# Optimization experiments

Measured on AMD Instinct MI355X. Metric: run time of the kernel, lower is better.

## Reference

```python
import jax, jax.numpy as jnp
import numpy as np

N_COMPRESS = 2048
N_EXPAND_QK = 1024
N_EXPAND_V = 1024
TOPK_C, TOPK_QK, TOPK_V = 8, 4, 6


def _topk_sparsify(w, k):
    # top-k along last dim, scatter back, renormalize (matches torch scatter_ path)
    vals, idx = jax.lax.top_k(w, k)                      # [B,k]
    rows = jnp.arange(w.shape[0])[:, None]
    sparse = jnp.zeros_like(w).at[rows, idx].set(vals)   # [B,N]
    return sparse / (sparse.sum(axis=-1, keepdims=True) + 1e-8)


def setup_inputs() -> dict:
    key = jax.random.key(0)
    k0, k1, k2, k3 = jax.random.split(key, 4)
    B, S, D, DS = 4, 4096, 2048, 64
    total = N_COMPRESS + N_EXPAND_QK + N_EXPAND_V
    return {
        "x": jax.random.normal(k0, (B, S, D), jnp.float32),
        "importance": jax.random.uniform(k1, (B, S), jnp.float32),
        "W": jax.random.normal(k2, (D, DS), jnp.float32) * 0.02,
        "b": jnp.zeros((DS,), jnp.float32),
        "neuron_emb": jax.random.normal(k3, (total, DS), jnp.float32) * 0.02,
    }


def reference(x, importance, W, b, neuron_emb):
    # projection (dropout is identity in eval mode)
    h = x @ W + b                                             # [B,S,ds]
    # cosine logits against unit-norm neuron embeddings
    emb_n = neuron_emb / jnp.linalg.norm(neuron_emb, axis=-1, keepdims=True)
    all_logits = jnp.einsum('bsd,nd->bsn', h, emb_n)          # [B,S,total]
    lC = all_logits[..., :N_COMPRESS]
    lQK = all_logits[..., N_COMPRESS:N_COMPRESS + N_EXPAND_QK]
    lV = all_logits[..., N_COMPRESS + N_EXPAND_QK:]
    pC = jax.nn.softmax(lC, axis=-1)
    pQK = jax.nn.softmax(lQK, axis=-1)   # expand_Q and expand_K share the slice (eval: identical)
    pV = jax.nn.softmax(lV, axis=-1)
    # importance-weighted pooling to per-batch dense routing weights
    dC = jnp.einsum('bs,bsn->bn', importance, pC)
    dQK = jnp.einsum('bs,bsn->bn', importance, pQK)
    dV = jnp.einsum('bs,bsn->bn', importance, pV)
    wC = _topk_sparsify(dC, TOPK_C)
    wQ = _topk_sparsify(dQK, TOPK_QK)
    wK = _topk_sparsify(dQK, TOPK_QK)
    wV = _topk_sparsify(dV, TOPK_V)
    # concat the four routing-weight outputs: [B, 2048+1024+1024+1024]
    return jnp.concatenate([wC, wQ, wK, wV], axis=-1)
```

## Files before the change

### kernel.cpp

```cpp
#include <hip/hip_runtime.h>
#include <math.h>

#define D_IN   2048

typedef __bf16 bf16x8 __attribute__((ext_vector_type(8)));
typedef float  f32x4  __attribute__((ext_vector_type(4)));

#define mfma16 __builtin_amdgcn_mfma_f32_16x16x32_bf16

__global__ __launch_bounds__(256) void k_prep(const float* __restrict__ emb,
                                              const float* __restrict__ W,
                                              __bf16* __restrict__ e_hi,
                                              __bf16* __restrict__ e_lo,
                                              __bf16* __restrict__ wt_hi,
                                              __bf16* __restrict__ wt_lo,
                                              float* __restrict__ dacc) {
    int blk = blockIdx.x, t = threadIdx.x;
    if (blk < 1024) {
        int gid  = blk * 256 + t;
        int row  = gid >> 6;
        int lane = gid & 63;
        float v  = emb[row * 64 + lane];
        float ss = v * v;
#pragma unroll
        for (int m = 32; m >= 1; m >>= 1) ss += __shfl_xor(ss, m);
        float nv = v / sqrtf(ss);
        __bf16 hb = (__bf16)nv;
        e_hi[row * 64 + lane] = hb;
        e_lo[row * 64 + lane] = (__bf16)(nv - (float)hb);
    } else if (blk < 1536) {
        int gid = (blk - 1024) * 256 + t;
        int c   = gid >> 11;
        int k   = gid & 2047;
        float v = W[k * 64 + c];
        __bf16 hb = (__bf16)v;
        wt_hi[c * 2048 + k] = hb;
        wt_lo[c * 2048 + k] = (__bf16)(v - (float)hb);
    } else {
        dacc[(blk - 1536) * 256 + t] = 0.f;
    }
}

__global__ __launch_bounds__(512, 4) void k_fused(
        const float* __restrict__ x,
        const __bf16* __restrict__ wt_hi, const __bf16* __restrict__ wt_lo,
        const float* __restrict__ bias,
        const __bf16* __restrict__ e_hi, const __bf16* __restrict__ e_lo,
        const float* __restrict__ imp, float* __restrict__ dacc) {
    __shared__ float  h_acc[32][66];
    __shared__ __bf16 hb_hi[32][64];
    __shared__ __bf16 hb_lo[32][64];
    __shared__ float  zs[8][4][8];

    int t    = threadIdx.x;
    int wave = t >> 6;
    int lane = t & 63;
    int l15  = lane & 15;
    int kg   = lane >> 4;
    int row0 = blockIdx.x * 32;
    const f32x4 z4 = {0.f, 0.f, 0.f, 0.f};

    for (int i = t; i < 32 * 66; i += 512) ((float*)h_acc)[i] = 0.f;
    __syncthreads();

    {
        f32x4 hacc[2][4];
#pragma unroll
        for (int rt = 0; rt < 2; ++rt)
#pragma unroll
            for (int ct = 0; ct < 4; ++ct) hacc[rt][ct] = z4;
        int kb0 = wave * 256;
        const float* xr0 = x + (size_t)(row0 + l15) * D_IN + kb0 + kg * 8;
        const float* xr1 = xr0 + 16 * D_IN;
        float4 xe0, xe1, xe2, xe3, xo0, xo1, xo2, xo3;

#define LDX(B, KS) { B##0 = *(const float4*)(xr0 + (KS) * 32); \
                     B##1 = *(const float4*)(xr0 + (KS) * 32 + 4); \
                     B##2 = *(const float4*)(xr1 + (KS) * 32); \
                     B##3 = *(const float4*)(xr1 + (KS) * 32 + 4); }
#define CVT8(DH, DL, V0, V1) { \
    float av[8] = {V0.x, V0.y, V0.z, V0.w, V1.x, V1.y, V1.z, V1.w}; \
    _Pragma("unroll") for (int j = 0; j < 8; ++j) { \
        __bf16 hb = (__bf16)av[j]; DH[j] = hb; \
        DL[j] = (__bf16)(av[j] - (float)hb); } }
#define HCOMP(B, KS) { \
    bf16x8 ah[2], al[2], bw[4]; \
    CVT8(ah[0], al[0], B##0, B##1) \
    CVT8(ah[1], al[1], B##2, B##3) \
    int kb = kb0 + (KS) * 32 + kg * 8; \
    _Pragma("unroll") for (int ct = 0; ct < 4; ++ct) \
        bw[ct] = *(const bf16x8*)(wt_hi + (size_t)(ct * 16 + l15) * D_IN + kb); \
    _Pragma("unroll") for (int rt = 0; rt < 2; ++rt) \
    _Pragma("unroll") for (int ct = 0; ct < 4; ++ct) \
        hacc[rt][ct] = mfma16(ah[rt], bw[ct], hacc[rt][ct], 0, 0, 0); \
    _Pragma("unroll") for (int rt = 0; rt < 2; ++rt) \
    _Pragma("unroll") for (int ct = 0; ct < 4; ++ct) \
        hacc[rt][ct] = mfma16(al[rt], bw[ct], hacc[rt][ct], 0, 0, 0); \
    _Pragma("unroll") for (int ct = 0; ct < 4; ++ct) \
        bw[ct] = *(const bf16x8*)(wt_lo + (size_t)(ct * 16 + l15) * D_IN + kb); \
    _Pragma("unroll") for (int rt = 0; rt < 2; ++rt) \
    _Pragma("unroll") for (int ct = 0; ct < 4; ++ct) \
        hacc[rt][ct] = mfma16(ah[rt], bw[ct], hacc[rt][ct], 0, 0, 0); }

        LDX(xe, 0)
        LDX(xo, 1) HCOMP(xe, 0)
        LDX(xe, 2) HCOMP(xo, 1)
        LDX(xo, 3) HCOMP(xe, 2)
        LDX(xe, 4) HCOMP(xo, 3)
        LDX(xo, 5) HCOMP(xe, 4)
        LDX(xe, 6) HCOMP(xo, 5)
        LDX(xo, 7) HCOMP(xe, 6)
        HCOMP(xo, 7)
#undef LDX
#undef HCOMP

#pragma unroll
        for (int rt = 0; rt < 2; ++rt)
#pragma unroll
            for (int ct = 0; ct < 4; ++ct)
#pragma unroll
                for (int r = 0; r < 4; ++r)
                    atomicAdd(&h_acc[rt * 16 + kg * 4 + r][ct * 16 + l15],
                              hacc[rt][ct][r]);
    }
    __syncthreads();
    if (wave == 0) {
#pragma unroll 4
        for (int row = 0; row < 32; ++row) {
            float v = h_acc[row][lane] + bias[lane];
            __bf16 hb = (__bf16)v;
            int c2 = ((((lane >> 3) ^ (row & 7)) << 3) | (lane & 7));
            hb_hi[row][c2] = hb;
            hb_lo[row][c2] = (__bf16)(v - (float)hb);
        }
    }
    __syncthreads();

    bf16x8 a_hi[2][2], a_lo[2][2];
#pragma unroll
    for (int rt = 0; rt < 2; ++rt)
#pragma unroll
        for (int ks = 0; ks < 2; ++ks) {
            int row = rt * 16 + l15;
            int g   = ((ks * 4 + kg) ^ (l15 & 7)) * 8;
            a_hi[rt][ks] = *(const bf16x8*)&hb_hi[row][g];
            a_lo[rt][ks] = *(const bf16x8*)&hb_lo[row][g];
        }

    int bb = blockIdx.x >> 7;
    float* dbase = dacc + bb * 4096;
    const __bf16* pe_hi = e_hi + l15 * 64 + kg * 8;
    const __bf16* pe_lo = e_lo + l15 * 64 + kg * 8;

#define LOADH(P, NN) { size_t off = (size_t)(NN) * 64; \
    P##H0 = *(const bf16x8*)(pe_hi + off); \
    P##H1 = *(const bf16x8*)(pe_hi + off + 32); \
    P##L0 = *(const bf16x8*)(pe_lo + off); \
    P##L1 = *(const bf16x8*)(pe_lo + off + 32); }
#define MFMAH(P, CT) { \
    _Pragma("unroll") for (int rt = 0; rt < 2; ++rt) { \
        f32x4 tt = acc[rt][CT]; \
        tt = mfma16(a_hi[rt][0], P##H0, tt, 0, 0, 0); \
        tt = mfma16(a_hi[rt][1], P##H1, tt, 0, 0, 0); \
        tt = mfma16(a_lo[rt][0], P##H0, tt, 0, 0, 0); \
        tt = mfma16(a_lo[rt][1], P##H1, tt, 0, 0, 0); \
        tt = mfma16(a_hi[rt][0], P##L0, tt, 0, 0, 0); \
        tt = mfma16(a_hi[rt][1], P##L1, tt, 0, 0, 0); \
        acc[rt][CT] = tt; } }

    bf16x8 qaH0, qaH1, qaL0, qaL1, qbH0, qbH1, qbL0, qbL1;

    const int segB[4] = {0, 2048, 3072, 4096};
    for (int sg = 0; sg < 3; ++sg) {
        int sBeg = segB[sg];
        int nc   = (segB[sg + 1] - sBeg) >> 8;
        float zc[2][4] = {};
        {
            LOADH(qa, sBeg + wave * 32)
            for (int c = 0; c < nc; ++c) {
                int n0 = sBeg + c * 256 + wave * 32;
                f32x4 acc[2][2];
                acc[0][0] = z4; acc[0][1] = z4; acc[1][0] = z4; acc[1][1] = z4;
                LOADH(qb, n0 + 16)
                MFMAH(qa, 0)
                if (c + 1 < nc) { LOADH(qa, n0 + 256) }
                MFMAH(qb, 1)
#pragma unroll
                for (int rt = 0; rt < 2; ++rt)
#pragma unroll
                    for (int r = 0; r < 4; ++r)
                        zc[rt][r] += __expf(acc[rt][0][r]) + __expf(acc[rt][1][r]);
            }
        }
#pragma unroll
        for (int rt = 0; rt < 2; ++rt)
#pragma unroll
            for (int r = 0; r < 4; ++r) {
                float z = zc[rt][r];
#pragma unroll
                for (int m = 1; m < 16; m <<= 1) z += __shfl_xor(z, m);
                zc[rt][r] = z;
            }
        if (l15 == 0) {
#pragma unroll
            for (int rt = 0; rt < 2; ++rt)
#pragma unroll
                for (int r = 0; r < 4; ++r)
                    zs[wave][kg][rt * 4 + r] = zc[rt][r];
        }
        __syncthreads();
        float cf[2][4];
#pragma unroll
        for (int rt = 0; rt < 2; ++rt)
#pragma unroll
            for (int r = 0; r < 4; ++r) {
                float z = 0.f;
#pragma unroll
                for (int w = 0; w < 8; ++w) z += zs[w][kg][rt * 4 + r];
                cf[rt][r] = imp[row0 + rt * 16 + kg * 4 + r] / z;
            }
        __syncthreads();
        {
            LOADH(qa, sBeg + wave * 32)
            for (int c = 0; c < nc; ++c) {
                int n0 = sBeg + c * 256 + wave * 32;
                f32x4 acc[2][2];
                acc[0][0] = z4; acc[0][1] = z4; acc[1][0] = z4; acc[1][1] = z4;
                LOADH(qb, n0 + 16)
                MFMAH(qa, 0)
                if (c + 1 < nc) { LOADH(qa, n0 + 256) }
                MFMAH(qb, 1)
                float s0 = 0.f, s1 = 0.f;
#pragma unroll
                for (int rt = 0; rt < 2; ++rt)
#pragma unroll
                    for (int r = 0; r < 4; ++r) {
                        s0 += cf[rt][r] * __expf(acc[rt][0][r]);
                        s1 += cf[rt][r] * __expf(acc[rt][1][r]);
                    }
                s0 += __shfl_xor(s0, 16); s0 += __shfl_xor(s0, 32);
                s1 += __shfl_xor(s1, 16); s1 += __shfl_xor(s1, 32);
                if (kg == 0) {
                    atomicAdd(&dbase[n0 + l15],      s0);
                    atomicAdd(&dbase[n0 + 16 + l15], s1);
                }
            }
        }
    }
#undef LOADH
#undef MFMAH
}

__global__ __launch_bounds__(256) void k_topk(const float* __restrict__ dacc,
                                              float* __restrict__ out) {
    __shared__ float dv[2048];
    __shared__ float redv[4];
    __shared__ int   redi[4];
    __shared__ float selv[8];
    __shared__ int   seli[8];
    int blk = blockIdx.x;
    int b   = blk / 3;
    int sg  = blk - 3 * b;
    int t   = threadIdx.x;
    const int segStart[3] = {0, 2048, 3072};
    const int segLen[3]   = {2048, 1024, 1024};
    const int segK[3]     = {8, 4, 6};
    const int segOut[3]   = {0, 2048, 4096};
    int st = segStart[sg], len = segLen[sg], kk = segK[sg];
    for (int n = t; n < len; n += 256) dv[n] = dacc[b * 4096 + st + n];
    __syncthreads();
    for (int it = 0; it < kk; ++it) {
        float bv = -3.0e38f;
        int   bi = 1 << 30;
        for (int n = t; n < len; n += 256) {
            float v = dv[n];
            if (v > bv) { bv = v; bi = n; }
        }
#pragma unroll
        for (int m = 1; m < 64; m <<= 1) {
            float ov = __shfl_xor(bv, m);
            int   oi = __shfl_xor(bi, m);
            if (ov > bv || (ov == bv && oi < bi)) { bv = ov; bi = oi; }
        }
        if ((t & 63) == 0) { redv[t >> 6] = bv; redi[t >> 6] = bi; }
        __syncthreads();
        if (t == 0) {
            for (int w = 1; w < 4; ++w)
                if (redv[w] > bv || (redv[w] == bv && redi[w] < bi)) {
                    bv = redv[w]; bi = redi[w];
                }
            selv[it] = bv;
            seli[it] = bi;
            dv[bi] = -3.4e38f;
        }
        __syncthreads();
    }
    float sum = 0.f;
    for (int it = 0; it < kk; ++it) sum += selv[it];
    float inv = 1.0f / (sum + 1e-8f);
    for (int n = t; n < len; n += 256) {
        float v = 0.0f;
        for (int it = 0; it < kk; ++it)
            if (seli[it] == n) v = selv[it] * inv;
        out[b * 5120 + segOut[sg] + n] = v;
        if (sg == 1) out[b * 5120 + 3072 + n] = v;
    }
}

extern "C" void kernel_launch(void* const* d_in, const int* in_sizes, int n_in,
                              void* d_out, int out_size, void* d_ws, size_t ws_size,
                              hipStream_t stream) {
    (void)in_sizes; (void)n_in; (void)out_size; (void)ws_size;
    const float* x    = (const float*)d_in[0];
    const float* imp  = (const float*)d_in[1];
    const float* W    = (const float*)d_in[2];
    const float* bias = (const float*)d_in[3];
    const float* emb  = (const float*)d_in[4];
    float* out = (float*)d_out;

    char* w = (char*)d_ws;
    __bf16* e_hi  = (__bf16*)w;  w += (size_t)4096 * 64 * 2;
    __bf16* e_lo  = (__bf16*)w;  w += (size_t)4096 * 64 * 2;
    __bf16* wt_hi = (__bf16*)w;  w += (size_t)64 * 2048 * 2;
    __bf16* wt_lo = (__bf16*)w;  w += (size_t)64 * 2048 * 2;
    float*  dacc  = (float*)w;   w += (size_t)4 * 4096 * 4;

    hipLaunchKernelGGL(k_prep,  dim3(1600), dim3(256), 0, stream,
                       emb, W, e_hi, e_lo, wt_hi, wt_lo, dacc);
    hipLaunchKernelGGL(k_fused, dim3(512),  dim3(512), 0, stream,
                       x, wt_hi, wt_lo, bias, e_hi, e_lo, imp, dacc);
    hipLaunchKernelGGL(k_topk,  dim3(12),   dim3(256), 0, stream,
                       dacc, out);
}
```

Before: 363.2 us.

## Halve rows per block to 16 and double grid for more parallelism

Each fused block now handles 16 token rows instead of 32, so the grid doubles from 512 to 1024 blocks and launch bounds ask for higher occupancy. Register state per thread shrinks (one row tile instead of two), and the manual software prefetch of embedding fragments is replaced by a simpler loop with unroll 2. The aim is to fill the 256 CUs more evenly and hide latency through occupancy. In exchange each block reloads the full embedding table for half as many rows, doubling embedding traffic and the number of atomic adds into the pooled accumulator.

```diff
diff --git a/kernel.cpp b/kernel.cpp
--- a/kernel.cpp
+++ b/kernel.cpp
@@ -41,66 +41,57 @@
     }
 }
 
-__global__ __launch_bounds__(512, 4) void k_fused(
+__global__ __launch_bounds__(512, 8) void k_fused(
         const float* __restrict__ x,
         const __bf16* __restrict__ wt_hi, const __bf16* __restrict__ wt_lo,
         const float* __restrict__ bias,
         const __bf16* __restrict__ e_hi, const __bf16* __restrict__ e_lo,
         const float* __restrict__ imp, float* __restrict__ dacc) {
-    __shared__ float  h_acc[32][66];
-    __shared__ __bf16 hb_hi[32][64];
-    __shared__ __bf16 hb_lo[32][64];
-    __shared__ float  zs[8][4][8];
+    __shared__ float  h_acc[16][66];
+    __shared__ __bf16 hb_hi[16][64];
+    __shared__ __bf16 hb_lo[16][64];
+    __shared__ float  zs[8][4][4];
 
     int t    = threadIdx.x;
     int wave = t >> 6;
     int lane = t & 63;
     int l15  = lane & 15;
     int kg   = lane >> 4;
-    int row0 = blockIdx.x * 32;
+    int row0 = blockIdx.x * 16;
     const f32x4 z4 = {0.f, 0.f, 0.f, 0.f};
 
-    for (int i = t; i < 32 * 66; i += 512) ((float*)h_acc)[i] = 0.f;
+    for (int i = t; i < 16 * 66; i += 512) ((float*)h_acc)[i] = 0.f;
     __syncthreads();
 
     {
-        f32x4 hacc[2][4];
-#pragma unroll
-        for (int rt = 0; rt < 2; ++rt)
-#pragma unroll
-            for (int ct = 0; ct < 4; ++ct) hacc[rt][ct] = z4;
+        f32x4 hacc[4];
+#pragma unroll
+        for (int ct = 0; ct < 4; ++ct) hacc[ct] = z4;
         int kb0 = wave * 256;
         const float* xr0 = x + (size_t)(row0 + l15) * D_IN + kb0 + kg * 8;
-        const float* xr1 = xr0 + 16 * D_IN;
-        float4 xe0, xe1, xe2, xe3, xo0, xo1, xo2, xo3;
+        float4 xe0, xe1, xo0, xo1;
 
 #define LDX(B, KS) { B##0 = *(const float4*)(xr0 + (KS) * 32); \
-                     B##1 = *(const float4*)(xr0 + (KS) * 32 + 4); \
-                     B##2 = *(const float4*)(xr1 + (KS) * 32); \
-                     B##3 = *(const float4*)(xr1 + (KS) * 32 + 4); }
+                     B##1 = *(const float4*)(xr0 + (KS) * 32 + 4); }
 #define CVT8(DH, DL, V0, V1) { \
     float av[8] = {V0.x, V0.y, V0.z, V0.w, V1.x, V1.y, V1.z, V1.w}; \
     _Pragma("unroll") for (int j = 0; j < 8; ++j) { \
         __bf16 hb = (__bf16)av[j]; DH[j] = hb; \
         DL[j] = (__bf16)(av[j] - (float)hb); } }
 #define HCOMP(B, KS) { \
-    bf16x8 ah[2], al[2], bw[4]; \
-    CVT8(ah[0], al[0], B##0, B##1) \
-    CVT8(ah[1], al[1], B##2, B##3) \
+    bf16x8 ah, al, bw[4]; \
+    CVT8(ah, al, B##0, B##1) \
     int kb = kb0 + (KS) * 32 + kg * 8; \
     _Pragma("unroll") for (int ct = 0; ct < 4; ++ct) \
         bw[ct] = *(const bf16x8*)(wt_hi + (size_t)(ct * 16 + l15) * D_IN + kb); \
-    _Pragma("unroll") for (int rt = 0; rt < 2; ++rt) \
-    _Pragma("unroll") for (int ct = 0; ct < 4; ++ct) \
-        hacc[rt][ct] = mfma16(ah[rt], bw[ct], hacc[rt][ct], 0, 0, 0); \
-    _Pragma("unroll") for (int rt = 0; rt < 2; ++rt) \
-    _Pragma("unroll") for (int ct = 0; ct < 4; ++ct) \
-        hacc[rt][ct] = mfma16(al[rt], bw[ct], hacc[rt][ct], 0, 0, 0); \
+    _Pragma("unroll") for (int ct = 0; ct < 4; ++ct) \
+        hacc[ct] = mfma16(ah, bw[ct], hacc[ct], 0, 0, 0); \
+    _Pragma("unroll") for (int ct = 0; ct < 4; ++ct) \
+        hacc[ct] = mfma16(al, bw[ct], hacc[ct], 0, 0, 0); \
     _Pragma("unroll") for (int ct = 0; ct < 4; ++ct) \
         bw[ct] = *(const bf16x8*)(wt_lo + (size_t)(ct * 16 + l15) * D_IN + kb); \
-    _Pragma("unroll") for (int rt = 0; rt < 2; ++rt) \
-    _Pragma("unroll") for (int ct = 0; ct < 4; ++ct) \
-        hacc[rt][ct] = mfma16(ah[rt], bw[ct], hacc[rt][ct], 0, 0, 0); }
+    _Pragma("unroll") for (int ct = 0; ct < 4; ++ct) \
+        hacc[ct] = mfma16(ah, bw[ct], hacc[ct], 0, 0, 0); }
 
         LDX(xe, 0)
         LDX(xo, 1) HCOMP(xe, 0)
@@ -112,21 +103,19 @@
         LDX(xo, 7) HCOMP(xe, 6)
         HCOMP(xo, 7)
 #undef LDX
+#undef CVT8
 #undef HCOMP
 
 #pragma unroll
-        for (int rt = 0; rt < 2; ++rt)
-#pragma unroll
-            for (int ct = 0; ct < 4; ++ct)
-#pragma unroll
-                for (int r = 0; r < 4; ++r)
-                    atomicAdd(&h_acc[rt * 16 + kg * 4 + r][ct * 16 + l15],
-                              hacc[rt][ct][r]);
+        for (int ct = 0; ct < 4; ++ct)
+#pragma unroll
+            for (int r = 0; r < 4; ++r)
+                atomicAdd(&h_acc[kg * 4 + r][ct * 16 + l15], hacc[ct][r]);
     }
     __syncthreads();
     if (wave == 0) {
 #pragma unroll 4
-        for (int row = 0; row < 32; ++row) {
+        for (int row = 0; row < 16; ++row) {
             float v = h_acc[row][lane] + bias[lane];
             __bf16 hb = (__bf16)v;
             int c2 = ((((lane >> 3) ^ (row & 7)) << 3) | (lane & 7));
@@ -136,119 +125,88 @@
     }
     __syncthreads();
 
-    bf16x8 a_hi[2][2], a_lo[2][2];
-#pragma unroll
-    for (int rt = 0; rt < 2; ++rt)
-#pragma unroll
-        for (int ks = 0; ks < 2; ++ks) {
-            int row = rt * 16 + l15;
-            int g   = ((ks * 4 + kg) ^ (l15 & 7)) * 8;
-            a_hi[rt][ks] = *(const bf16x8*)&hb_hi[row][g];
-            a_lo[rt][ks] = *(const bf16x8*)&hb_lo[row][g];
-        }
-
-    int bb = blockIdx.x >> 7;
+    bf16x8 a_hi[2], a_lo[2];
+#pragma unroll
+    for (int ks = 0; ks < 2; ++ks) {
+        int g = ((ks * 4 + kg) ^ (l15 & 7)) * 8;
+        a_hi[ks] = *(const bf16x8*)&hb_hi[l15][g];
+        a_lo[ks] = *(const bf16x8*)&hb_lo[l15][g];
+    }
+
+    int bb = blockIdx.x >> 8;
     float* dbase = dacc + bb * 4096;
-    const __bf16* pe_hi = e_hi + l15 * 64 + kg * 8;
-    const __bf16* pe_lo = e_lo + l15 * 64 + kg * 8;
-
-#define LOADH(P, NN) { size_t off = (size_t)(NN) * 64; \
-    P##H0 = *(const bf16x8*)(pe_hi + off); \
-    P##H1 = *(const bf16x8*)(pe_hi + off + 32); \
-    P##L0 = *(const bf16x8*)(pe_lo + off); \
-    P##L1 = *(const bf16x8*)(pe_lo + off + 32); }
-#define MFMAH(P, CT) { \
-    _Pragma("unroll") for (int rt = 0; rt < 2; ++rt) { \
-        f32x4 tt = acc[rt][CT]; \
-        tt = mfma16(a_hi[rt][0], P##H0, tt, 0, 0, 0); \
-        tt = mfma16(a_hi[rt][1], P##H1, tt, 0, 0, 0); \
-        tt = mfma16(a_lo[rt][0], P##H0, tt, 0, 0, 0); \
-        tt = mfma16(a_lo[rt][1], P##H1, tt, 0, 0, 0); \
-        tt = mfma16(a_hi[rt][0], P##L0, tt, 0, 0, 0); \
-        tt = mfma16(a_hi[rt][1], P##L1, tt, 0, 0, 0); \
-        acc[rt][CT] = tt; } }
-
-    bf16x8 qaH0, qaH1, qaL0, qaL1, qbH0, qbH1, qbL0, qbL1;
+
+#define DOT16(ACC, NN) { \
+    const __bf16* eh = e_hi + (size_t)((NN) + l15) * 64 + kg * 8; \
+    const __bf16* el = e_lo + (size_t)((NN) + l15) * 64 + kg * 8; \
+    bf16x8 h0 = *(const bf16x8*)eh; \
+    bf16x8 h1 = *(const bf16x8*)(eh + 32); \
+    bf16x8 l0 = *(const bf16x8*)el; \
+    bf16x8 l1 = *(const bf16x8*)(el + 32); \
+    ACC = mfma16(a_hi[0], h0, ACC, 0, 0, 0); \
+    ACC = mfma16(a_hi[1], h1, ACC, 0, 0, 0); \
+    ACC = mfma16(a_lo[0], h0, ACC, 0, 0, 0); \
+    ACC = mfma16(a_lo[1], h1, ACC, 0, 0, 0); \
+    ACC = mfma16(a_hi[0], l0, ACC, 0, 0, 0); \
+    ACC = mfma16(a_hi[1], l1, ACC, 0, 0, 0); }
 
     const int segB[4] = {0, 2048, 3072, 4096};
     for (int sg = 0; sg < 3; ++sg) {
         int sBeg = segB[sg];
         int nc   = (segB[sg + 1] - sBeg) >> 8;
-        float zc[2][4] = {};
-        {
-            LOADH(qa, sBeg + wave * 32)
-            for (int c = 0; c < nc; ++c) {
-                int n0 = sBeg + c * 256 + wave * 32;
-                f32x4 acc[2][2];
-                acc[0][0] = z4; acc[0][1] = z4; acc[1][0] = z4; acc[1][1] = z4;
-                LOADH(qb, n0 + 16)
-                MFMAH(qa, 0)
-                if (c + 1 < nc) { LOADH(qa, n0 + 256) }
-                MFMAH(qb, 1)
-#pragma unroll
-                for (int rt = 0; rt < 2; ++rt)
-#pragma unroll
-                    for (int r = 0; r < 4; ++r)
-                        zc[rt][r] += __expf(acc[rt][0][r]) + __expf(acc[rt][1][r]);
+        float zc[4] = {};
+#pragma unroll 2
+        for (int c = 0; c < nc; ++c) {
+            int n0 = sBeg + c * 256 + wave * 32;
+            f32x4 acc0 = z4, acc1 = z4;
+            DOT16(acc0, n0)
+            DOT16(acc1, n0 + 16)
+#pragma unroll
+            for (int r = 0; r < 4; ++r)
+                zc[r] += __expf(acc0[r]) + __expf(acc1[r]);
+        }
+#pragma unroll
+        for (int r = 0; r < 4; ++r) {
+            float z = zc[r];
+#pragma unroll
+            for (int m = 1; m < 16; m <<= 1) z += __shfl_xor(z, m);
+            zc[r] = z;
+        }
+        if (l15 == 0) {
+#pragma unroll
+            for (int r = 0; r < 4; ++r) zs[wave][kg][r] = zc[r];
+        }
+        __syncthreads();
+        float cf[4];
+#pragma unroll
+        for (int r = 0; r < 4; ++r) {
+            float z = 0.f;
+#pragma unroll
+            for (int w = 0; w < 8; ++w) z += zs[w][kg][r];
+            cf[r] = imp[row0 + kg * 4 + r] / z;
+        }
+        __syncthreads();
+#pragma unroll 2
+        for (int c = 0; c < nc; ++c) {
+            int n0 = sBeg + c * 256 + wave * 32;
+            f32x4 acc0 = z4, acc1 = z4;
+            DOT16(acc0, n0)
+            DOT16(acc1, n0 + 16)
+            float s0 = 0.f, s1 = 0.f;
+#pragma unroll
+            for (int r = 0; r < 4; ++r) {
+                s0 += cf[r] * __expf(acc0[r]);
+                s1 += cf[r] * __expf(acc1[r]);
             }
-        }
-#pragma unroll
-        for (int rt = 0; rt < 2; ++rt)
-#pragma unroll
-            for (int r = 0; r < 4; ++r) {
-                float z = zc[rt][r];
-#pragma unroll
-                for (int m = 1; m < 16; m <<= 1) z += __shfl_xor(z, m);
-                zc[rt][r] = z;
+            s0 += __shfl_xor(s0, 16); s0 += __shfl_xor(s0, 32);
+            s1 += __shfl_xor(s1, 16); s1 += __shfl_xor(s1, 32);
+            if (kg == 0) {
+                atomicAdd(&dbase[n0 + l15],      s0);
+                atomicAdd(&dbase[n0 + 16 + l15], s1);
             }
-        if (l15 == 0) {
-#pragma unroll
-            for (int rt = 0; rt < 2; ++rt)
-#pragma unroll
-                for (int r = 0; r < 4; ++r)
-                    zs[wave][kg][rt * 4 + r] = zc[rt][r];
-        }
-        __syncthreads();
-        float cf[2][4];
-#pragma unroll
-        for (int rt = 0; rt < 2; ++rt)
-#pragma unroll
-            for (int r = 0; r < 4; ++r) {
-                float z = 0.f;
-#pragma unroll
-                for (int w = 0; w < 8; ++w) z += zs[w][kg][rt * 4 + r];
-                cf[rt][r] = imp[row0 + rt * 16 + kg * 4 + r] / z;
-            }
-        __syncthreads();
-        {
-            LOADH(qa, sBeg + wave * 32)
-            for (int c = 0; c < nc; ++c) {
-                int n0 = sBeg + c * 256 + wave * 32;
-                f32x4 acc[2][2];
-                acc[0][0] = z4; acc[0][1] = z4; acc[1][0] = z4; acc[1][1] = z4;
-                LOADH(qb, n0 + 16)
-                MFMAH(qa, 0)
-                if (c + 1 < nc) { LOADH(qa, n0 + 256) }
-                MFMAH(qb, 1)
-                float s0 = 0.f, s1 = 0.f;
-#pragma unroll
-                for (int rt = 0; rt < 2; ++rt)
-#pragma unroll
-                    for (int r = 0; r < 4; ++r) {
-                        s0 += cf[rt][r] * __expf(acc[rt][0][r]);
-                        s1 += cf[rt][r] * __expf(acc[rt][1][r]);
-                    }
-                s0 += __shfl_xor(s0, 16); s0 += __shfl_xor(s0, 32);
-                s1 += __shfl_xor(s1, 16); s1 += __shfl_xor(s1, 32);
-                if (kg == 0) {
-                    atomicAdd(&dbase[n0 + l15],      s0);
-                    atomicAdd(&dbase[n0 + 16 + l15], s1);
-                }
-            }
-        }
-    }
-#undef LOADH
-#undef MFMAH
+        }
+    }
+#undef DOT16
 }
 
 __global__ __launch_bounds__(256) void k_topk(const float* __restrict__ dacc,
@@ -327,7 +285,7 @@
 
     hipLaunchKernelGGL(k_prep,  dim3(1600), dim3(256), 0, stream,
                        emb, W, e_hi, e_lo, wt_hi, wt_lo, dacc);
-    hipLaunchKernelGGL(k_fused, dim3(512),  dim3(512), 0, stream,
+    hipLaunchKernelGGL(k_fused, dim3(1024), dim3(512), 0, stream,
                        x, wt_hi, wt_lo, bias, e_hi, e_lo, imp, dacc);
     hipLaunchKernelGGL(k_topk,  dim3(12),   dim3(256), 0, stream,
                        dacc, out);
```

Result: slower. 492.5 us (+35.6%).
